# Kernel optimization log

Hardware: AMD Instinct MI355X
Metric: run time of the kernel (lower is better)

## Reference

```python
import jax, jax.numpy as jnp
import numpy as np

B, S, D = 4, 2048, 512
H = 8
DK = D // H
DFF = 2048
EPS = 1e-5


def _layernorm(x, g, b):
    mu = jnp.mean(x, axis=-1, keepdims=True)
    var = jnp.mean((x - mu) ** 2, axis=-1, keepdims=True)
    return (x - mu) * jax.lax.rsqrt(var + EPS) * g + b


def setup_inputs() -> dict:
    key = jax.random.key(0)
    ks = jax.random.split(key, 12)
    s = 1.0 / np.sqrt(D)
    sf = 1.0 / np.sqrt(DFF)
    return {
        "x": jax.random.normal(ks[0], (B, S, D), dtype=jnp.float32),
        "Wq": jax.random.uniform(ks[1], (D, D), jnp.float32, -s, s),
        "bq": jnp.zeros((D,), jnp.float32),
        "Wk": jax.random.uniform(ks[2], (D, D), jnp.float32, -s, s),
        "bk": jnp.zeros((D,), jnp.float32),
        "Wv": jax.random.uniform(ks[3], (D, D), jnp.float32, -s, s),
        "bv": jnp.zeros((D,), jnp.float32),
        "Wo": jax.random.uniform(ks[4], (D, D), jnp.float32, -s, s),
        "bo": jnp.zeros((D,), jnp.float32),
        "W1": jax.random.uniform(ks[5], (D, DFF), jnp.float32, -s, s),
        "b1": jnp.zeros((DFF,), jnp.float32),
        "W2": jax.random.uniform(ks[6], (DFF, D), jnp.float32, -sf, sf),
        "b2": jnp.zeros((D,), jnp.float32),
        "g1": jnp.ones((D,), jnp.float32),
        "be1": jnp.zeros((D,), jnp.float32),
        "g2": jnp.ones((D,), jnp.float32),
        "be2": jnp.zeros((D,), jnp.float32),
    }


def reference(x, Wq, bq, Wk, bk, Wv, bv, Wo, bo, W1, b1, W2, b2, g1, be1, g2, be2):
    # Multi-head attention (dropout = identity at eval)
    def heads(v):  # [B,S,D] -> [B,H,S,DK]
        return v.reshape(B, S, H, DK).transpose(0, 2, 1, 3)

    q = heads(x @ Wq + bq)
    k = heads(x @ Wk + bk)
    v = heads(x @ Wv + bv)
    scores = jnp.einsum("bhsd,bhtd->bhst", q, k) / np.sqrt(DK)
    attn = jax.nn.softmax(scores, axis=-1)
    ctx = jnp.einsum("bhst,bhtd->bhsd", attn, v)
    ctx = ctx.transpose(0, 2, 1, 3).reshape(B, S, D)
    attn_out = ctx @ Wo + bo

    x1 = _layernorm(x + attn_out, g1, be1)

    ff = jax.nn.relu(x1 @ W1 + b1) @ W2 + b2
    return _layernorm(x1 + ff, g2, be2)
```

## Files before the change

### kernel.cpp

```cpp
#include <hip/hip_runtime.h>
#include <hip/hip_bf16.h>
#include <stdint.h>

typedef __bf16 bf16;
typedef __attribute__((ext_vector_type(8))) __bf16 bf16x8;
typedef __attribute__((ext_vector_type(4))) float f32x4;

#define DEVI __device__ __forceinline__

constexpr int Bz = 4, Sz = 2048, Dz = 512, Hz = 8, DKz = 64, DFFz = 2048;
constexpr int ROWSz = Bz * Sz;
constexpr float EPSf = 1e-5f;
constexpr float C2f = 0.125f * 1.44269504088896f;

DEVI void load_lds16(void* lds, const void* g) {
  __builtin_amdgcn_global_load_lds(
      (const __attribute__((address_space(1))) void*)(uintptr_t)(g),
      (__attribute__((address_space(3))) void*)(uint32_t)(uintptr_t)(lds),
      16, 0, 0);
}

template <int BM, int EPI>
__global__ __launch_bounds__(256) void gemm_bt(
    const bf16* __restrict__ A, const bf16* __restrict__ Bt,
    const float* __restrict__ bias, const float* __restrict__ resid,
    const bf16* __restrict__ residb, bf16* __restrict__ aux,
    void* __restrict__ Cout, int M, int N, int K) {
  constexpr int BN = 128, BK = 64;
  constexpr int MI = BM / 32;
  __shared__ alignas(16) bf16 sA[2][BM * BK];
  __shared__ alignas(16) bf16 sB[2][BN * BK];
  const int tid = threadIdx.x;
  const int lane = tid & 63;
  const int wv = tid >> 6;
  const int n0 = blockIdx.x * BN;
  const int m0 = blockIdx.y * BM;

  const int srow = lane >> 3;
  const int sch = ((lane & 7) ^ srow) * 8;
  const bf16* gA = A + (size_t)(m0 + wv * (BM / 4) + srow) * K + sch;
  const bf16* gB = Bt + (size_t)(n0 + wv * 32 + srow) * K + sch;

  const int wm = (wv >> 1) * (BM / 2);
  const int wn = (wv & 1) * 64;
  const int fr = lane & 15;
  const int fq = lane >> 4;

  auto stage = [&](int buf, int k0) {
#pragma unroll
    for (int j = 0; j < BM / 32; ++j)
      load_lds16(sA[buf] + (wv * (BM / 4) + j * 8) * BK, gA + (size_t)(j * 8) * K + k0);
#pragma unroll
    for (int j = 0; j < 4; ++j)
      load_lds16(sB[buf] + (wv * 32 + j * 8) * BK, gB + (size_t)(j * 8) * K + k0);
  };

  f32x4 acc[MI][4] = {};

  stage(0, 0);
  __syncthreads();

  const int niter = K / BK;
  for (int it = 0; it < niter; ++it) {
    const int cur = it & 1;
    if (it + 1 < niter) stage(cur ^ 1, (it + 1) * BK);
#pragma unroll
    for (int kk = 0; kk < 2; ++kk) {
      const int fc = ((4 * kk + fq) ^ (fr & 7)) * 8;
      bf16x8 af[MI], bfr[4];
#pragma unroll
      for (int i = 0; i < MI; ++i)
        af[i] = *(const bf16x8*)(sA[cur] + (wm + i * 16 + fr) * BK + fc);
#pragma unroll
      for (int j = 0; j < 4; ++j)
        bfr[j] = *(const bf16x8*)(sB[cur] + (wn + j * 16 + fr) * BK + fc);
#pragma unroll
      for (int i = 0; i < MI; ++i)
#pragma unroll
        for (int j = 0; j < 4; ++j)
          acc[i][j] = __builtin_amdgcn_mfma_f32_16x16x32_bf16(af[i], bfr[j], acc[i][j], 0, 0, 0);
    }
    __syncthreads();
  }

#pragma unroll
  for (int i = 0; i < MI; ++i) {
#pragma unroll
    for (int j = 0; j < 4; ++j) {
      const int col = n0 + wn + j * 16 + fr;
      const float bv = bias[col];
      if (EPI == 3 && col >= 1024) {
        const int row0 = m0 + wm + i * 16 + fq * 4;
        const int hh = (col - 1024) >> 6, dk = (col - 1024) & 63;
        const int bb = row0 >> 11, s0 = row0 & 2047;
        bf16 pv[4];
#pragma unroll
        for (int r = 0; r < 4; ++r) pv[r] = (bf16)(acc[i][j][r] + bv);
        *(uint2*)(aux + (size_t)((bb * 8 + hh) * 64 + dk) * 2048 + s0) = *(const uint2*)pv;
      } else {
#pragma unroll
        for (int r = 0; r < 4; ++r) {
          const int row = m0 + wm + i * 16 + fq * 4 + r;
          const size_t idx = (size_t)row * N + col;
          float v = acc[i][j][r] + bv;
          if (EPI == 1) {
            ((bf16*)Cout)[idx] = (bf16)(v + resid[idx]);
          } else if (EPI == 2) {
            ((bf16*)Cout)[idx] = (bf16)(v > 0.f ? v : 0.f);
          } else if (EPI == 3) {
            ((bf16*)Cout)[idx] = (bf16)(col < 512 ? v * C2f : v);
          } else {
            ((bf16*)Cout)[idx] = (bf16)(v + (float)residb[idx]);
          }
        }
      }
    }
  }
}

__global__ __launch_bounds__(256, 2) void flash_attn(
    const bf16* __restrict__ qkv, const bf16* __restrict__ Vt,
    bf16* __restrict__ ctx) {
  const int bid = blockIdx.x;
  const int qt = bid & 15;
  const int h = (bid >> 4) & 7;
  const int b = bid >> 7;
  const int q0 = qt * 128;
  const int tid = threadIdx.x, lane = tid & 63, wv = tid >> 6;
  const int fr = lane & 15, fq = lane >> 4;
  const int xsw = fr & 7;

  __shared__ alignas(16) bf16 sK[2][64 * 64];
  __shared__ alignas(16) bf16 sV[2][64 * 64];
  __shared__ alignas(16) bf16 sP[128 * 64];

  const int srow = lane >> 3;
  const int scol = ((lane & 7) ^ srow) * 8;

  const bf16* gQ = qkv + (size_t)(b * Sz + q0 + wv * 32 + srow) * 1536 + h * 64 + scol;
  const bf16* gK = qkv + (size_t)(b * Sz + wv * 16 + srow) * 1536 + 512 + h * 64 + scol;
  const bf16* gV = Vt + (size_t)((b * 8 + h) * 64 + wv * 16 + srow) * Sz + scol;

#pragma unroll
  for (int i = 0; i < 4; ++i)
    load_lds16(sP + (wv * 32 + i * 8) * 64, gQ + (size_t)(i * 8) * 1536);
  load_lds16(sK[0] + (wv * 16 + 0) * 64, gK);
  load_lds16(sK[0] + (wv * 16 + 8) * 64, gK + (size_t)8 * 1536);
  load_lds16(sV[0] + (wv * 16 + 0) * 64, gV);
  load_lds16(sV[0] + (wv * 16 + 8) * 64, gV + (size_t)8 * Sz);
  asm volatile("s_waitcnt vmcnt(0)" ::: "memory");
  __syncthreads();

  const int colc0 = (fq ^ xsw) * 8;
  const int colc1 = ((fq + 4) ^ xsw) * 8;
  int pcol[4], qsrc[4];
#pragma unroll
  for (int j = 0; j < 4; ++j)
    pcol[j] = (((fq + 4 * j) >> 1) ^ xsw) * 8 + (fq & 1) * 4;
#pragma unroll
  for (int r = 0; r < 4; ++r) qsrc[r] = (fq * 4 + r) | (lane & 48);

  bf16x8 qb[2][2];
#pragma unroll
  for (int s = 0; s < 2; ++s) {
    qb[s][0] = *(const bf16x8*)(sP + (wv * 32 + s * 16 + fr) * 64 + colc0);
    qb[s][1] = *(const bf16x8*)(sP + (wv * 32 + s * 16 + fr) * 64 + colc1);
  }
  asm volatile("s_waitcnt lgkmcnt(0)" ::: "memory");

  float l_part[2] = {0.f, 0.f};
  f32x4 acc_o[2][4] = {};

  for (int it = 0; it < 32; ++it) {
    const int cur = it & 1;
    if (it + 1 < 32) {
      const int nxt = cur ^ 1;
      const size_t t1 = (size_t)(it + 1) * 64;
      load_lds16(sK[nxt] + (wv * 16 + 0) * 64, gK + t1 * 1536);
      load_lds16(sK[nxt] + (wv * 16 + 8) * 64, gK + (t1 + 8) * 1536);
      load_lds16(sV[nxt] + (wv * 16 + 0) * 64, gV + t1);
      load_lds16(sV[nxt] + (wv * 16 + 8) * 64, gV + (size_t)8 * Sz + t1);
    }

    bf16x8 kf[2][4];
#pragma unroll
    for (int j = 0; j < 4; ++j) {
      kf[0][j] = *(const bf16x8*)(sK[cur] + (j * 16 + fr) * 64 + colc0);
      kf[1][j] = *(const bf16x8*)(sK[cur] + (j * 16 + fr) * 64 + colc1);
    }
    f32x4 sc[2][4] = {};
#pragma unroll
    for (int s = 0; s < 2; ++s)
#pragma unroll
      for (int kk = 0; kk < 2; ++kk)
#pragma unroll
        for (int j = 0; j < 4; ++j)
          sc[s][j] = __builtin_amdgcn_mfma_f32_16x16x32_bf16(kf[kk][j], qb[s][kk], sc[s][j], 0, 0, 0);

#pragma unroll
    for (int s = 0; s < 2; ++s) {
      float rs = 0.f;
#pragma unroll
      for (int j = 0; j < 4; ++j) {
        float e0 = __builtin_amdgcn_exp2f(sc[s][j][0]);
        float e1 = __builtin_amdgcn_exp2f(sc[s][j][1]);
        float e2 = __builtin_amdgcn_exp2f(sc[s][j][2]);
        float e3 = __builtin_amdgcn_exp2f(sc[s][j][3]);
        rs += (e0 + e1) + (e2 + e3);
        bf16 pt[4] = {(bf16)e0, (bf16)e1, (bf16)e2, (bf16)e3};
        *(uint2*)(sP + (wv * 32 + s * 16 + fr) * 64 + pcol[j]) = *(const uint2*)pt;
      }
      l_part[s] += rs;
    }
    asm volatile("s_waitcnt lgkmcnt(0)" ::: "memory");

    bf16x8 vf[2][4];
#pragma unroll
    for (int j = 0; j < 4; ++j) {
      vf[0][j] = *(const bf16x8*)(sV[cur] + (j * 16 + fr) * 64 + colc0);
      vf[1][j] = *(const bf16x8*)(sV[cur] + (j * 16 + fr) * 64 + colc1);
    }
#pragma unroll
    for (int s = 0; s < 2; ++s)
#pragma unroll
      for (int kk = 0; kk < 2; ++kk) {
        bf16x8 ap = *(const bf16x8*)(sP + (wv * 32 + s * 16 + fr) * 64 + (kk ? colc1 : colc0));
#pragma unroll
        for (int j = 0; j < 4; ++j)
          acc_o[s][j] = __builtin_amdgcn_mfma_f32_16x16x32_bf16(ap, vf[kk][j], acc_o[s][j], 0, 0, 0);
      }
    __syncthreads();
  }

#pragma unroll
  for (int s = 0; s < 2; ++s) {
    float l = l_part[s];
    l += __shfl_xor(l, 16, 64);
    l += __shfl_xor(l, 32, 64);
    float rl[4];
#pragma unroll
    for (int r = 0; r < 4; ++r) rl[r] = 1.0f / __shfl(l, qsrc[r], 64);
#pragma unroll
    for (int j = 0; j < 4; ++j)
#pragma unroll
      for (int r = 0; r < 4; ++r) {
        const int row = b * Sz + q0 + wv * 32 + s * 16 + fq * 4 + r;
        const int col = h * 64 + j * 16 + fr;
        ctx[(size_t)row * Dz + col] = (bf16)(acc_o[s][j][r] * rl[r]);
      }
  }
}

template <int OUT_F32>
__global__ __launch_bounds__(256) void layer_norm_k(
    const bf16* __restrict__ y, const float* __restrict__ g,
    const float* __restrict__ be, void* __restrict__ out) {
  const int row = blockIdx.x * 4 + (threadIdx.x >> 6);
  const int lane = threadIdx.x & 63;
  const int col = lane * 8;
  bf16x8 hv = *(const bf16x8*)(y + (size_t)row * Dz + col);
  float v[8];
  float s = 0.f, ss = 0.f;
#pragma unroll
  for (int i = 0; i < 8; ++i) {
    v[i] = (float)hv[i];
    s += v[i];
    ss += v[i] * v[i];
  }
#pragma unroll
  for (int o = 1; o < 64; o <<= 1) {
    s += __shfl_xor(s, o, 64);
    ss += __shfl_xor(ss, o, 64);
  }
  const float mu = s * (1.0f / Dz);
  const float rstd = rsqrtf(ss * (1.0f / Dz) - mu * mu + EPSf);
  const float4* g4 = (const float4*)(g + col);
  const float4* b4 = (const float4*)(be + col);
  float4 ga = g4[0], gb = g4[1], ba = b4[0], bb = b4[1];
  float o8[8];
  o8[0] = (v[0] - mu) * rstd * ga.x + ba.x;
  o8[1] = (v[1] - mu) * rstd * ga.y + ba.y;
  o8[2] = (v[2] - mu) * rstd * ga.z + ba.z;
  o8[3] = (v[3] - mu) * rstd * ga.w + ba.w;
  o8[4] = (v[4] - mu) * rstd * gb.x + bb.x;
  o8[5] = (v[5] - mu) * rstd * gb.y + bb.y;
  o8[6] = (v[6] - mu) * rstd * gb.z + bb.z;
  o8[7] = (v[7] - mu) * rstd * gb.w + bb.w;
  if (OUT_F32) {
    float4* of = (float4*)((float*)out + (size_t)row * Dz + col);
    of[0] = make_float4(o8[0], o8[1], o8[2], o8[3]);
    of[1] = make_float4(o8[4], o8[5], o8[6], o8[7]);
  } else {
    bf16 ob[8];
#pragma unroll
    for (int i = 0; i < 8; ++i) ob[i] = (bf16)o8[i];
    *(uint4*)((bf16*)out + (size_t)row * Dz + col) = *(const uint4*)ob;
  }
}

__global__ __launch_bounds__(256) void prep_all(
    const float* __restrict__ Wq, const float* __restrict__ Wk,
    const float* __restrict__ Wv, const float* __restrict__ Wo,
    const float* __restrict__ W1, const float* __restrict__ W2,
    const float* __restrict__ bq, const float* __restrict__ bk,
    const float* __restrict__ bv, const float* __restrict__ x,
    bf16* __restrict__ WqkvT, bf16* __restrict__ WoT,
    bf16* __restrict__ W1T, bf16* __restrict__ W2T,
    float* __restrict__ bqkv, bf16* __restrict__ xb) {
  __shared__ float tile[64][65];
  const int blk = blockIdx.x;
  const int t = threadIdx.x;
  if (blk < 768) {
    const float* W;
    bf16* Wt;
    int K, N, local;
    if (blk < 64)       { W = Wq; Wt = WqkvT;                       K = 512;  N = 512;  local = blk; }
    else if (blk < 128) { W = Wk; Wt = WqkvT + (size_t)512 * 512;   K = 512;  N = 512;  local = blk - 64; }
    else if (blk < 192) { W = Wv; Wt = WqkvT + (size_t)1024 * 512;  K = 512;  N = 512;  local = blk - 128; }
    else if (blk < 256) { W = Wo; Wt = WoT;                         K = 512;  N = 512;  local = blk - 192; }
    else if (blk < 512) { W = W1; Wt = W1T;                         K = 512;  N = 2048; local = blk - 256; }
    else                { W = W2; Wt = W2T;                         K = 2048; N = 512;  local = blk - 512; }
    const int kt = K / 64;
    const int k0 = (local % kt) * 64, n0 = (local / kt) * 64;
    const int r = t >> 2, c = (t & 3) * 16;
    const float* src = W + (size_t)(k0 + r) * N + n0 + c;
#pragma unroll
    for (int i = 0; i < 4; ++i) {
      float4 v = ((const float4*)src)[i];
      tile[r][c + i * 4 + 0] = v.x;
      tile[r][c + i * 4 + 1] = v.y;
      tile[r][c + i * 4 + 2] = v.z;
      tile[r][c + i * 4 + 3] = v.w;
    }
    __syncthreads();
    union { bf16 hh[16]; uint4 u[2]; } pk;
#pragma unroll
    for (int i = 0; i < 16; ++i) pk.hh[i] = (bf16)tile[c + i][r];
    uint4* dst = (uint4*)(Wt + (size_t)(n0 + r) * K + k0 + c);
    dst[0] = pk.u[0];
    dst[1] = pk.u[1];
  } else if (blk == 768) {
    for (int i = t; i < 1536; i += 256)
      bqkv[i] = i < 512 ? bq[i] : (i < 1024 ? bk[i - 512] : bv[i - 1024]);
  } else {
    const int local = blk - 769;
#pragma unroll
    for (int k = 0; k < 4; ++k) {
      const int i = local * 1024 + k * 256 + t;
      float4 v = ((const float4*)x)[i];
      bf16 tv[4] = {(bf16)v.x, (bf16)v.y, (bf16)v.z, (bf16)v.w};
      ((uint2*)xb)[i] = *(const uint2*)tv;
    }
  }
}

extern "C" void kernel_launch(void* const* d_in, const int* in_sizes, int n_in,
                              void* d_out, int out_size, void* d_ws, size_t ws_size,
                              hipStream_t stream) {
  const float* x   = (const float*)d_in[0];
  const float* Wq  = (const float*)d_in[1];
  const float* bq  = (const float*)d_in[2];
  const float* Wk  = (const float*)d_in[3];
  const float* bk  = (const float*)d_in[4];
  const float* Wv  = (const float*)d_in[5];
  const float* bvp = (const float*)d_in[6];
  const float* Wo  = (const float*)d_in[7];
  const float* bo  = (const float*)d_in[8];
  const float* W1  = (const float*)d_in[9];
  const float* b1  = (const float*)d_in[10];
  const float* W2  = (const float*)d_in[11];
  const float* b2  = (const float*)d_in[12];
  const float* g1  = (const float*)d_in[13];
  const float* be1 = (const float*)d_in[14];
  const float* g2  = (const float*)d_in[15];
  const float* be2 = (const float*)d_in[16];

  char* ws = (char*)d_ws;
  size_t off = 0;
  auto alloc = [&](size_t bytes) -> void* {
    void* p = ws + off;
    off += (bytes + 255) & ~(size_t)255;
    return p;
  };
  bf16*  WqkvT = (bf16*)alloc((size_t)1536 * 512 * 2);
  float* bqkv  = (float*)alloc(1536 * 4);
  bf16*  WoT   = (bf16*)alloc((size_t)512 * 512 * 2);
  bf16*  W1T   = (bf16*)alloc((size_t)2048 * 512 * 2);
  bf16*  W2T   = (bf16*)alloc((size_t)512 * 2048 * 2);
  bf16*  xb    = (bf16*)alloc((size_t)ROWSz * 512 * 2);
  bf16*  qkv   = (bf16*)alloc((size_t)ROWSz * 1536 * 2);
  bf16*  Vt    = (bf16*)alloc((size_t)32 * 64 * 2048 * 2);
  bf16*  ctx   = (bf16*)alloc((size_t)ROWSz * 512 * 2);
  bf16*  y1    = (bf16*)alloc((size_t)ROWSz * 512 * 2);
  bf16*  x1b   = (bf16*)alloc((size_t)ROWSz * 512 * 2);
  bf16*  hbuf  = qkv;
  bf16*  y2    = y1;

  prep_all<<<dim3(1793), 256, 0, stream>>>(Wq, Wk, Wv, Wo, W1, W2, bq, bk, bvp, x,
                                           WqkvT, WoT, W1T, W2T, bqkv, xb);

  gemm_bt<128, 3><<<dim3(12, 64), 256, 0, stream>>>(xb, WqkvT, bqkv, nullptr, nullptr, Vt, qkv, ROWSz, 1536, 512);
  flash_attn<<<dim3(512), 256, 0, stream>>>(qkv, Vt, ctx);
  gemm_bt<64, 1><<<dim3(4, 128), 256, 0, stream>>>(ctx, WoT, bo, x, nullptr, nullptr, y1, ROWSz, 512, 512);
  layer_norm_k<0><<<dim3(2048), 256, 0, stream>>>(y1, g1, be1, x1b);
  gemm_bt<128, 2><<<dim3(16, 64), 256, 0, stream>>>(x1b, W1T, b1, nullptr, nullptr, nullptr, hbuf, ROWSz, 2048, 512);
  gemm_bt<64, 4><<<dim3(4, 128), 256, 0, stream>>>(hbuf, W2T, b2, nullptr, x1b, nullptr, y2, ROWSz, 512, 2048);
  layer_norm_k<1><<<dim3(2048), 256, 0, stream>>>(y2, g2, be2, d_out);
}
```

Before: 246.2 us.

## Add BK template to GEMM, raise occupancy bounds, halve flash-attn block size

The GEMM kernel gets a BK template parameter, with a BK=32 path (new swizzle and staging layout) used for the two BM=128 GEMMs, and min-blocks launch bounds are added to shrink LDS and register use so more blocks fit per CU. Flash attention now uses 128-thread blocks with 64 query rows each and twice as many blocks, and K/V staging is rewritten so two waves load whole tiles. The aim is more concurrent work per CU and better latency hiding. In exchange the GEMM runs more K iterations and barriers, and attention reloads K/V once per 64 query rows instead of per 128, doubling that global traffic.

Result: slower. 251.2 us (+2.0%).

```diff
diff --git a/kernel.cpp b/kernel.cpp
--- a/kernel.cpp
+++ b/kernel.cpp
@@ -20,14 +20,17 @@
       16, 0, 0);
 }
 
-template <int BM, int EPI>
-__global__ __launch_bounds__(256) void gemm_bt(
+template <int BM, int BK, int EPI>
+__global__ __launch_bounds__(256, BM == 128 ? 4 : 3) void gemm_bt(
     const bf16* __restrict__ A, const bf16* __restrict__ Bt,
     const float* __restrict__ bias, const float* __restrict__ resid,
     const bf16* __restrict__ residb, bf16* __restrict__ aux,
     void* __restrict__ Cout, int M, int N, int K) {
-  constexpr int BN = 128, BK = 64;
+  constexpr int BN = 128;
   constexpr int MI = BM / 32;
+  constexpr int RPI = 512 / BK;
+  constexpr int AISS = (BM / 4) / RPI;
+  constexpr int BISS = 32 / RPI;
   __shared__ alignas(16) bf16 sA[2][BM * BK];
   __shared__ alignas(16) bf16 sB[2][BN * BK];
   const int tid = threadIdx.x;
@@ -36,8 +39,9 @@
   const int n0 = blockIdx.x * BN;
   const int m0 = blockIdx.y * BM;
 
-  const int srow = lane >> 3;
-  const int sch = ((lane & 7) ^ srow) * 8;
+  const int srow = (BK == 32) ? (lane >> 2) : (lane >> 3);
+  const int sch = (BK == 32) ? (((lane & 3) ^ (srow & 3)) * 8)
+                             : (((lane & 7) ^ (srow & 7)) * 8);
   const bf16* gA = A + (size_t)(m0 + wv * (BM / 4) + srow) * K + sch;
   const bf16* gB = Bt + (size_t)(n0 + wv * 32 + srow) * K + sch;
 
@@ -48,11 +52,11 @@
 
   auto stage = [&](int buf, int k0) {
 #pragma unroll
-    for (int j = 0; j < BM / 32; ++j)
-      load_lds16(sA[buf] + (wv * (BM / 4) + j * 8) * BK, gA + (size_t)(j * 8) * K + k0);
-#pragma unroll
-    for (int j = 0; j < 4; ++j)
-      load_lds16(sB[buf] + (wv * 32 + j * 8) * BK, gB + (size_t)(j * 8) * K + k0);
+    for (int j = 0; j < AISS; ++j)
+      load_lds16(sA[buf] + (wv * (BM / 4) + j * RPI) * BK, gA + (size_t)(j * RPI) * K + k0);
+#pragma unroll
+    for (int j = 0; j < BISS; ++j)
+      load_lds16(sB[buf] + (wv * 32 + j * RPI) * BK, gB + (size_t)(j * RPI) * K + k0);
   };
 
   f32x4 acc[MI][4] = {};
@@ -65,8 +69,9 @@
     const int cur = it & 1;
     if (it + 1 < niter) stage(cur ^ 1, (it + 1) * BK);
 #pragma unroll
-    for (int kk = 0; kk < 2; ++kk) {
-      const int fc = ((4 * kk + fq) ^ (fr & 7)) * 8;
+    for (int kk = 0; kk < BK / 32; ++kk) {
+      const int fc = (BK == 32) ? ((fq ^ (fr & 3)) * 8)
+                                : (((4 * kk + fq) ^ (fr & 7)) * 8);
       bf16x8 af[MI], bfr[4];
 #pragma unroll
       for (int i = 0; i < MI; ++i)
@@ -118,36 +123,41 @@
   }
 }
 
-__global__ __launch_bounds__(256, 2) void flash_attn(
+__global__ __launch_bounds__(128, 2) void flash_attn(
     const bf16* __restrict__ qkv, const bf16* __restrict__ Vt,
     bf16* __restrict__ ctx) {
   const int bid = blockIdx.x;
-  const int qt = bid & 15;
-  const int h = (bid >> 4) & 7;
-  const int b = bid >> 7;
-  const int q0 = qt * 128;
+  const int qt = bid & 31;
+  const int h = (bid >> 5) & 7;
+  const int b = bid >> 8;
+  const int q0 = qt * 64;
   const int tid = threadIdx.x, lane = tid & 63, wv = tid >> 6;
   const int fr = lane & 15, fq = lane >> 4;
   const int xsw = fr & 7;
 
   __shared__ alignas(16) bf16 sK[2][64 * 64];
   __shared__ alignas(16) bf16 sV[2][64 * 64];
-  __shared__ alignas(16) bf16 sP[128 * 64];
+  __shared__ alignas(16) bf16 sP[64 * 64];
 
   const int srow = lane >> 3;
   const int scol = ((lane & 7) ^ srow) * 8;
 
   const bf16* gQ = qkv + (size_t)(b * Sz + q0 + wv * 32 + srow) * 1536 + h * 64 + scol;
-  const bf16* gK = qkv + (size_t)(b * Sz + wv * 16 + srow) * 1536 + 512 + h * 64 + scol;
-  const bf16* gV = Vt + (size_t)((b * 8 + h) * 64 + wv * 16 + srow) * Sz + scol;
+  const bf16* gK = qkv + (size_t)(b * Sz + wv * 32 + srow) * 1536 + 512 + h * 64 + scol;
+  const bf16* gV = Vt + (size_t)((b * 8 + h) * 64 + wv * 32 + srow) * Sz + scol;
+
+  auto stageKV = [&](int buf, size_t t0) {
+#pragma unroll
+    for (int j = 0; j < 4; ++j) {
+      load_lds16(sK[buf] + (wv * 32 + j * 8) * 64, gK + (t0 + j * 8) * 1536);
+      load_lds16(sV[buf] + (wv * 32 + j * 8) * 64, gV + (size_t)(j * 8) * Sz + t0);
+    }
+  };
 
 #pragma unroll
   for (int i = 0; i < 4; ++i)
     load_lds16(sP + (wv * 32 + i * 8) * 64, gQ + (size_t)(i * 8) * 1536);
-  load_lds16(sK[0] + (wv * 16 + 0) * 64, gK);
-  load_lds16(sK[0] + (wv * 16 + 8) * 64, gK + (size_t)8 * 1536);
-  load_lds16(sV[0] + (wv * 16 + 0) * 64, gV);
-  load_lds16(sV[0] + (wv * 16 + 8) * 64, gV + (size_t)8 * Sz);
+  stageKV(0, 0);
   asm volatile("s_waitcnt vmcnt(0)" ::: "memory");
   __syncthreads();
 
@@ -173,14 +183,7 @@
 
   for (int it = 0; it < 32; ++it) {
     const int cur = it & 1;
-    if (it + 1 < 32) {
-      const int nxt = cur ^ 1;
-      const size_t t1 = (size_t)(it + 1) * 64;
-      load_lds16(sK[nxt] + (wv * 16 + 0) * 64, gK + t1 * 1536);
-      load_lds16(sK[nxt] + (wv * 16 + 8) * 64, gK + (t1 + 8) * 1536);
-      load_lds16(sV[nxt] + (wv * 16 + 0) * 64, gV + t1);
-      load_lds16(sV[nxt] + (wv * 16 + 8) * 64, gV + (size_t)8 * Sz + t1);
-    }
+    if (it + 1 < 32) stageKV(cur ^ 1, (size_t)(it + 1) * 64);
 
     bf16x8 kf[2][4];
 #pragma unroll
@@ -399,11 +402,11 @@
   prep_all<<<dim3(1793), 256, 0, stream>>>(Wq, Wk, Wv, Wo, W1, W2, bq, bk, bvp, x,
                                            WqkvT, WoT, W1T, W2T, bqkv, xb);
 
-  gemm_bt<128, 3><<<dim3(12, 64), 256, 0, stream>>>(xb, WqkvT, bqkv, nullptr, nullptr, Vt, qkv, ROWSz, 1536, 512);
-  flash_attn<<<dim3(512), 256, 0, stream>>>(qkv, Vt, ctx);
-  gemm_bt<64, 1><<<dim3(4, 128), 256, 0, stream>>>(ctx, WoT, bo, x, nullptr, nullptr, y1, ROWSz, 512, 512);
+  gemm_bt<128, 32, 3><<<dim3(12, 64), 256, 0, stream>>>(xb, WqkvT, bqkv, nullptr, nullptr, Vt, qkv, ROWSz, 1536, 512);
+  flash_attn<<<dim3(1024), 128, 0, stream>>>(qkv, Vt, ctx);
+  gemm_bt<64, 64, 1><<<dim3(4, 128), 256, 0, stream>>>(ctx, WoT, bo, x, nullptr, nullptr, y1, ROWSz, 512, 512);
   layer_norm_k<0><<<dim3(2048), 256, 0, stream>>>(y1, g1, be1, x1b);
-  gemm_bt<128, 2><<<dim3(16, 64), 256, 0, stream>>>(x1b, W1T, b1, nullptr, nullptr, nullptr, hbuf, ROWSz, 2048, 512);
-  gemm_bt<64, 4><<<dim3(4, 128), 256, 0, stream>>>(hbuf, W2T, b2, nullptr, x1b, nullptr, y2, ROWSz, 512, 2048);
+  gemm_bt<128, 32, 2><<<dim3(16, 64), 256, 0, stream>>>(x1b, W1T, b1, nullptr, nullptr, nullptr, hbuf, ROWSz, 2048, 512);
+  gemm_bt<64, 64, 4><<<dim3(4, 128), 256, 0, stream>>>(hbuf, W2T, b2, nullptr, x1b, nullptr, y2, ROWSz, 512, 2048);
   layer_norm_k<1><<<dim3(2048), 256, 0, stream>>>(y2, g2, be2, d_out);
 }
```

## Use triple-buffered LDS pipelines with partial vmcnt waits in GEMM and attention

Applied to the files above, without the earlier changes.

Both the GEMM and the flash-attention kernels move from double to triple buffering. Each barrier now waits only for the older async global-to-LDS loads (vmcnt(N)) rather than draining every load, so two tiles stay in flight. In the GEMM, BK is halved to 32 to make room for the third LDS stage, the swizzle is adapted to match, and occupancy hints are added to launch_bounds. The cost is more iterations with more barriers per tile, extra LDS per block, and hand-counted vmcnt values that must match the number of loads issued.

After: 254.7 us. +3.4%, slower.

```diff
diff --git a/kernel.cpp b/kernel.cpp
--- a/kernel.cpp
+++ b/kernel.cpp
@@ -20,24 +20,38 @@
       16, 0, 0);
 }
 
+template <int N> DEVI void bar_keep() {
+  if constexpr (N == 2)
+    asm volatile("s_waitcnt vmcnt(2) lgkmcnt(0)\ns_barrier" ::: "memory");
+  else if constexpr (N == 3)
+    asm volatile("s_waitcnt vmcnt(3) lgkmcnt(0)\ns_barrier" ::: "memory");
+  else
+    asm volatile("s_waitcnt vmcnt(4) lgkmcnt(0)\ns_barrier" ::: "memory");
+}
+DEVI void bar_full() {
+  asm volatile("s_waitcnt vmcnt(0) lgkmcnt(0)\ns_barrier" ::: "memory");
+}
+
 template <int BM, int EPI>
-__global__ __launch_bounds__(256) void gemm_bt(
+__global__ __launch_bounds__(256, BM == 128 ? 3 : 4) void gemm_bt(
     const bf16* __restrict__ A, const bf16* __restrict__ Bt,
     const float* __restrict__ bias, const float* __restrict__ resid,
     const bf16* __restrict__ residb, bf16* __restrict__ aux,
     void* __restrict__ Cout, int M, int N, int K) {
-  constexpr int BN = 128, BK = 64;
+  constexpr int BN = 128, BK = 32;
   constexpr int MI = BM / 32;
-  __shared__ alignas(16) bf16 sA[2][BM * BK];
-  __shared__ alignas(16) bf16 sB[2][BN * BK];
+  constexpr int AISS = (BM / 4) / 16;
+  constexpr int ISS = AISS + 2;
+  __shared__ alignas(16) bf16 sA[3][BM * BK];
+  __shared__ alignas(16) bf16 sB[3][BN * BK];
   const int tid = threadIdx.x;
   const int lane = tid & 63;
   const int wv = tid >> 6;
   const int n0 = blockIdx.x * BN;
   const int m0 = blockIdx.y * BM;
 
-  const int srow = lane >> 3;
-  const int sch = ((lane & 7) ^ srow) * 8;
+  const int srow = lane >> 2;
+  const int sch = ((lane & 3) ^ (srow & 3)) * 8;
   const bf16* gA = A + (size_t)(m0 + wv * (BM / 4) + srow) * K + sch;
   const bf16* gB = Bt + (size_t)(n0 + wv * 32 + srow) * K + sch;
 
@@ -45,42 +59,52 @@
   const int wn = (wv & 1) * 64;
   const int fr = lane & 15;
   const int fq = lane >> 4;
-
-  auto stage = [&](int buf, int k0) {
-#pragma unroll
-    for (int j = 0; j < BM / 32; ++j)
-      load_lds16(sA[buf] + (wv * (BM / 4) + j * 8) * BK, gA + (size_t)(j * 8) * K + k0);
+  const int fc = (fq ^ (fr & 3)) * 8;
+
+  auto stage = [&](bf16* sa, bf16* sb, int k0) {
+#pragma unroll
+    for (int j = 0; j < AISS; ++j)
+      load_lds16(sa + (wv * (BM / 4) + j * 16) * BK, gA + (size_t)(j * 16) * K + k0);
+#pragma unroll
+    for (int j = 0; j < 2; ++j)
+      load_lds16(sb + (wv * 32 + j * 16) * BK, gB + (size_t)(j * 16) * K + k0);
+  };
+
+  f32x4 acc[MI][4] = {};
+  auto compute = [&](const bf16* sa, const bf16* sb) {
+    bf16x8 af[MI], bfr[4];
+#pragma unroll
+    for (int i = 0; i < MI; ++i)
+      af[i] = *(const bf16x8*)(sa + (wm + i * 16 + fr) * BK + fc);
 #pragma unroll
     for (int j = 0; j < 4; ++j)
-      load_lds16(sB[buf] + (wv * 32 + j * 8) * BK, gB + (size_t)(j * 8) * K + k0);
+      bfr[j] = *(const bf16x8*)(sb + (wn + j * 16 + fr) * BK + fc);
+#pragma unroll
+    for (int i = 0; i < MI; ++i)
+#pragma unroll
+      for (int j = 0; j < 4; ++j)
+        acc[i][j] = __builtin_amdgcn_mfma_f32_16x16x32_bf16(af[i], bfr[j], acc[i][j], 0, 0, 0);
   };
 
-  f32x4 acc[MI][4] = {};
-
-  stage(0, 0);
-  __syncthreads();
+  bf16 *sa0 = sA[0], *sa1 = sA[1], *sa2 = sA[2];
+  bf16 *sb0 = sB[0], *sb1 = sB[1], *sb2 = sB[2];
+
+  stage(sa0, sb0, 0);
+  stage(sa1, sb1, BK);
+  bar_keep<ISS>();
 
   const int niter = K / BK;
   for (int it = 0; it < niter; ++it) {
-    const int cur = it & 1;
-    if (it + 1 < niter) stage(cur ^ 1, (it + 1) * BK);
-#pragma unroll
-    for (int kk = 0; kk < 2; ++kk) {
-      const int fc = ((4 * kk + fq) ^ (fr & 7)) * 8;
-      bf16x8 af[MI], bfr[4];
-#pragma unroll
-      for (int i = 0; i < MI; ++i)
-        af[i] = *(const bf16x8*)(sA[cur] + (wm + i * 16 + fr) * BK + fc);
-#pragma unroll
-      for (int j = 0; j < 4; ++j)
-        bfr[j] = *(const bf16x8*)(sB[cur] + (wn + j * 16 + fr) * BK + fc);
-#pragma unroll
-      for (int i = 0; i < MI; ++i)
-#pragma unroll
-        for (int j = 0; j < 4; ++j)
-          acc[i][j] = __builtin_amdgcn_mfma_f32_16x16x32_bf16(af[i], bfr[j], acc[i][j], 0, 0, 0);
-    }
-    __syncthreads();
+    if (it + 2 < niter) {
+      stage(sa2, sb2, (it + 2) * BK);
+      compute(sa0, sb0);
+      bar_keep<ISS>();
+    } else {
+      compute(sa0, sb0);
+      bar_full();
+    }
+    bf16* ta = sa0; sa0 = sa1; sa1 = sa2; sa2 = ta;
+    bf16* tb = sb0; sb0 = sb1; sb1 = sb2; sb2 = tb;
   }
 
 #pragma unroll
@@ -130,8 +154,8 @@
   const int fr = lane & 15, fq = lane >> 4;
   const int xsw = fr & 7;
 
-  __shared__ alignas(16) bf16 sK[2][64 * 64];
-  __shared__ alignas(16) bf16 sV[2][64 * 64];
+  __shared__ alignas(16) bf16 sK[3][64 * 64];
+  __shared__ alignas(16) bf16 sV[3][64 * 64];
   __shared__ alignas(16) bf16 sP[128 * 64];
 
   const int srow = lane >> 3;
@@ -141,15 +165,22 @@
   const bf16* gK = qkv + (size_t)(b * Sz + wv * 16 + srow) * 1536 + 512 + h * 64 + scol;
   const bf16* gV = Vt + (size_t)((b * 8 + h) * 64 + wv * 16 + srow) * Sz + scol;
 
+  auto stageKV = [&](bf16* sk, bf16* sv, size_t t0) {
+    load_lds16(sk + (wv * 16 + 0) * 64, gK + t0 * 1536);
+    load_lds16(sk + (wv * 16 + 8) * 64, gK + (t0 + 8) * 1536);
+    load_lds16(sv + (wv * 16 + 0) * 64, gV + t0);
+    load_lds16(sv + (wv * 16 + 8) * 64, gV + (size_t)8 * Sz + t0);
+  };
+
+  bf16 *k0p = sK[0], *k1p = sK[1], *k2p = sK[2];
+  bf16 *v0p = sV[0], *v1p = sV[1], *v2p = sV[2];
+
 #pragma unroll
   for (int i = 0; i < 4; ++i)
     load_lds16(sP + (wv * 32 + i * 8) * 64, gQ + (size_t)(i * 8) * 1536);
-  load_lds16(sK[0] + (wv * 16 + 0) * 64, gK);
-  load_lds16(sK[0] + (wv * 16 + 8) * 64, gK + (size_t)8 * 1536);
-  load_lds16(sV[0] + (wv * 16 + 0) * 64, gV);
-  load_lds16(sV[0] + (wv * 16 + 8) * 64, gV + (size_t)8 * Sz);
-  asm volatile("s_waitcnt vmcnt(0)" ::: "memory");
-  __syncthreads();
+  stageKV(k0p, v0p, 0);
+  stageKV(k1p, v1p, 64);
+  bar_keep<4>();
 
   const int colc0 = (fq ^ xsw) * 8;
   const int colc1 = ((fq + 4) ^ xsw) * 8;
@@ -172,21 +203,14 @@
   f32x4 acc_o[2][4] = {};
 
   for (int it = 0; it < 32; ++it) {
-    const int cur = it & 1;
-    if (it + 1 < 32) {
-      const int nxt = cur ^ 1;
-      const size_t t1 = (size_t)(it + 1) * 64;
-      load_lds16(sK[nxt] + (wv * 16 + 0) * 64, gK + t1 * 1536);
-      load_lds16(sK[nxt] + (wv * 16 + 8) * 64, gK + (t1 + 8) * 1536);
-      load_lds16(sV[nxt] + (wv * 16 + 0) * 64, gV + t1);
-      load_lds16(sV[nxt] + (wv * 16 + 8) * 64, gV + (size_t)8 * Sz + t1);
-    }
+    const bool steady = (it + 2 < 32);
+    if (steady) stageKV(k2p, v2p, (size_t)(it + 2) * 64);
 
     bf16x8 kf[2][4];
 #pragma unroll
     for (int j = 0; j < 4; ++j) {
-      kf[0][j] = *(const bf16x8*)(sK[cur] + (j * 16 + fr) * 64 + colc0);
-      kf[1][j] = *(const bf16x8*)(sK[cur] + (j * 16 + fr) * 64 + colc1);
+      kf[0][j] = *(const bf16x8*)(k0p + (j * 16 + fr) * 64 + colc0);
+      kf[1][j] = *(const bf16x8*)(k0p + (j * 16 + fr) * 64 + colc1);
     }
     f32x4 sc[2][4] = {};
 #pragma unroll
@@ -217,8 +241,8 @@
     bf16x8 vf[2][4];
 #pragma unroll
     for (int j = 0; j < 4; ++j) {
-      vf[0][j] = *(const bf16x8*)(sV[cur] + (j * 16 + fr) * 64 + colc0);
-      vf[1][j] = *(const bf16x8*)(sV[cur] + (j * 16 + fr) * 64 + colc1);
+      vf[0][j] = *(const bf16x8*)(v0p + (j * 16 + fr) * 64 + colc0);
+      vf[1][j] = *(const bf16x8*)(v0p + (j * 16 + fr) * 64 + colc1);
     }
 #pragma unroll
     for (int s = 0; s < 2; ++s)
@@ -229,7 +253,10 @@
         for (int j = 0; j < 4; ++j)
           acc_o[s][j] = __builtin_amdgcn_mfma_f32_16x16x32_bf16(ap, vf[kk][j], acc_o[s][j], 0, 0, 0);
       }
-    __syncthreads();
+    if (steady) bar_keep<4>();
+    else bar_full();
+    bf16* tk = k0p; k0p = k1p; k1p = k2p; k2p = tk;
+    bf16* tv = v0p; v0p = v1p; v1p = v2p; v2p = tv;
   }
 
 #pragma unroll
```

## Parameterize GEMM K-tile, use BK=32 for wide GEMMs, bf16 residual for Wo

Applied to the files above, without the earlier changes.

Makes the GEMM K-tile size a template parameter, with a matching LDS swizzle for BK=32, and uses BK=32 for the QKV and W1 GEMMs. It also adds occupancy hints through launch_bounds min-blocks. The Wo GEMM epilogue now adds the bf16 copy of x as the residual instead of fp32 x. Smaller tiles cut LDS use so more blocks fit per CU, at the cost of more loop iterations and barriers. The bf16 residual loses some precision.

Result: no change. 243.6 us, median of 2 (-1.1%).

```diff
diff --git a/kernel.cpp b/kernel.cpp
--- a/kernel.cpp
+++ b/kernel.cpp
@@ -20,14 +20,17 @@
       16, 0, 0);
 }
 
-template <int BM, int EPI>
-__global__ __launch_bounds__(256) void gemm_bt(
+template <int BM, int BK, int EPI>
+__global__ __launch_bounds__(256, BM == 128 ? 4 : 3) void gemm_bt(
     const bf16* __restrict__ A, const bf16* __restrict__ Bt,
     const float* __restrict__ bias, const float* __restrict__ resid,
     const bf16* __restrict__ residb, bf16* __restrict__ aux,
     void* __restrict__ Cout, int M, int N, int K) {
-  constexpr int BN = 128, BK = 64;
+  constexpr int BN = 128;
   constexpr int MI = BM / 32;
+  constexpr int RPI = 512 / BK;
+  constexpr int AISS = (BM / 4) / RPI;
+  constexpr int BISS = 32 / RPI;
   __shared__ alignas(16) bf16 sA[2][BM * BK];
   __shared__ alignas(16) bf16 sB[2][BN * BK];
   const int tid = threadIdx.x;
@@ -36,8 +39,9 @@
   const int n0 = blockIdx.x * BN;
   const int m0 = blockIdx.y * BM;
 
-  const int srow = lane >> 3;
-  const int sch = ((lane & 7) ^ srow) * 8;
+  const int srow = (BK == 32) ? (lane >> 2) : (lane >> 3);
+  const int sch = (BK == 32) ? (((lane & 3) ^ (srow & 3)) * 8)
+                             : (((lane & 7) ^ (srow & 7)) * 8);
   const bf16* gA = A + (size_t)(m0 + wv * (BM / 4) + srow) * K + sch;
   const bf16* gB = Bt + (size_t)(n0 + wv * 32 + srow) * K + sch;
 
@@ -48,11 +52,11 @@
 
   auto stage = [&](int buf, int k0) {
 #pragma unroll
-    for (int j = 0; j < BM / 32; ++j)
-      load_lds16(sA[buf] + (wv * (BM / 4) + j * 8) * BK, gA + (size_t)(j * 8) * K + k0);
-#pragma unroll
-    for (int j = 0; j < 4; ++j)
-      load_lds16(sB[buf] + (wv * 32 + j * 8) * BK, gB + (size_t)(j * 8) * K + k0);
+    for (int j = 0; j < AISS; ++j)
+      load_lds16(sA[buf] + (wv * (BM / 4) + j * RPI) * BK, gA + (size_t)(j * RPI) * K + k0);
+#pragma unroll
+    for (int j = 0; j < BISS; ++j)
+      load_lds16(sB[buf] + (wv * 32 + j * RPI) * BK, gB + (size_t)(j * RPI) * K + k0);
   };
 
   f32x4 acc[MI][4] = {};
@@ -65,8 +69,9 @@
     const int cur = it & 1;
     if (it + 1 < niter) stage(cur ^ 1, (it + 1) * BK);
 #pragma unroll
-    for (int kk = 0; kk < 2; ++kk) {
-      const int fc = ((4 * kk + fq) ^ (fr & 7)) * 8;
+    for (int kk = 0; kk < BK / 32; ++kk) {
+      const int fc = (BK == 32) ? ((fq ^ (fr & 3)) * 8)
+                                : (((4 * kk + fq) ^ (fr & 7)) * 8);
       bf16x8 af[MI], bfr[4];
 #pragma unroll
       for (int i = 0; i < MI; ++i)
@@ -399,11 +404,11 @@
   prep_all<<<dim3(1793), 256, 0, stream>>>(Wq, Wk, Wv, Wo, W1, W2, bq, bk, bvp, x,
                                            WqkvT, WoT, W1T, W2T, bqkv, xb);
 
-  gemm_bt<128, 3><<<dim3(12, 64), 256, 0, stream>>>(xb, WqkvT, bqkv, nullptr, nullptr, Vt, qkv, ROWSz, 1536, 512);
+  gemm_bt<128, 32, 3><<<dim3(12, 64), 256, 0, stream>>>(xb, WqkvT, bqkv, nullptr, nullptr, Vt, qkv, ROWSz, 1536, 512);
   flash_attn<<<dim3(512), 256, 0, stream>>>(qkv, Vt, ctx);
-  gemm_bt<64, 1><<<dim3(4, 128), 256, 0, stream>>>(ctx, WoT, bo, x, nullptr, nullptr, y1, ROWSz, 512, 512);
+  gemm_bt<64, 64, 4><<<dim3(4, 128), 256, 0, stream>>>(ctx, WoT, bo, nullptr, xb, nullptr, y1, ROWSz, 512, 512);
   layer_norm_k<0><<<dim3(2048), 256, 0, stream>>>(y1, g1, be1, x1b);
-  gemm_bt<128, 2><<<dim3(16, 64), 256, 0, stream>>>(x1b, W1T, b1, nullptr, nullptr, nullptr, hbuf, ROWSz, 2048, 512);
-  gemm_bt<64, 4><<<dim3(4, 128), 256, 0, stream>>>(hbuf, W2T, b2, nullptr, x1b, nullptr, y2, ROWSz, 512, 2048);
+  gemm_bt<128, 32, 2><<<dim3(16, 64), 256, 0, stream>>>(x1b, W1T, b1, nullptr, nullptr, nullptr, hbuf, ROWSz, 2048, 512);
+  gemm_bt<64, 64, 4><<<dim3(4, 128), 256, 0, stream>>>(hbuf, W2T, b2, nullptr, x1b, nullptr, y2, ROWSz, 512, 2048);
   layer_norm_k<1><<<dim3(2048), 256, 0, stream>>>(y2, g2, be2, d_out);
 }
```
